# Kernel optimization log

Measured on AMD Instinct MI355X. Metric: run time of the kernel, lower is better.

## Reference

```python
import jax, jax.numpy as jnp
import numpy as np

N = 50000      # nodes
E = 800000     # directed edges (before self-loops)
IN = 128       # in_channels
H = 4          # heads (layers 1,2)
C = 64         # hidden_channels per head
OUT = 512      # out_channels of final Linear
LEAKY_SLOPE = 0.2


def _gat_layer(x, src, dst, n, W, a_src, a_dst, b, concat):
    """PyG GATConv (v1): shared linear, additive attention, segment softmax over dst."""
    heads, ch = a_src.shape
    xl = (x @ W).reshape(n, heads, ch)                       # [N,H,C]
    as_n = jnp.sum(xl * a_src, axis=-1)                      # [N,H] alpha_src per node
    ad_n = jnp.sum(xl * a_dst, axis=-1)                      # [N,H] alpha_dst per node
    logits = jax.nn.leaky_relu(as_n[src] + ad_n[dst], LEAKY_SLOPE)  # [Etot,H]
    m = jax.lax.stop_gradient(jax.ops.segment_max(logits, dst, num_segments=n))
    p = jnp.exp(logits - m[dst])
    denom = jax.ops.segment_sum(p, dst, num_segments=n) + 1e-16
    alpha = p / denom[dst]                                   # segment softmax over incoming edges
    out = jax.ops.segment_sum(xl[src] * alpha[:, :, None], dst, num_segments=n)  # [N,H,C]
    out = out.reshape(n, heads * ch) if concat else out.mean(axis=1)
    return out + b


def setup_inputs() -> dict:
    key = jax.random.key(0)
    ks = jax.random.split(key, 16)

    def gl(k, shape, fan_in):
        return jax.random.normal(k, shape, dtype=jnp.float32) * np.float32(1.0 / np.sqrt(fan_in))

    x = jax.random.normal(ks[0], (N, IN), dtype=jnp.float32)
    edge_index = jax.random.randint(ks[1], (2, E), 0, N, dtype=jnp.int32)

    inp = {
        "x": x,
        "edge_index": edge_index,
        # layer 1: in -> H*C (concat)
        "W1": gl(ks[2], (IN, H * C), IN),
        "a_src1": gl(ks[3], (H, C), C),
        "a_dst1": gl(ks[4], (H, C), C),
        "b1": jnp.zeros((H * C,), jnp.float32),
        # layer 2: H*C -> H*C (concat)
        "W2": gl(ks[5], (H * C, H * C), H * C),
        "a_src2": gl(ks[6], (H, C), C),
        "a_dst2": gl(ks[7], (H, C), C),
        "b2": jnp.zeros((H * C,), jnp.float32),
        # layer 3: H*C -> C (1 head, no concat)
        "W3": gl(ks[8], (H * C, C), H * C),
        "a_src3": gl(ks[9], (1, C), C),
        "a_dst3": gl(ks[10], (1, C), C),
        "b3": jnp.zeros((C,), jnp.float32),
        # final fc: C -> OUT
        "Wfc": gl(ks[11], (C, OUT), C),
        "bfc": jnp.zeros((OUT,), jnp.float32),
    }
    return inp


def reference(x, edge_index, W1, a_src1, a_dst1, b1, W2, a_src2, a_dst2, b2,
              W3, a_src3, a_dst3, b3, Wfc, bfc):
    n = x.shape[0]
    loop = jnp.arange(n, dtype=edge_index.dtype)             # PyG GATConv adds self-loops
    src = jnp.concatenate([edge_index[0], loop])
    dst = jnp.concatenate([edge_index[1], loop])

    h = jax.nn.relu(_gat_layer(x, src, dst, n, W1, a_src1, a_dst1, b1, True))
    h = jax.nn.relu(_gat_layer(h, src, dst, n, W2, a_src2, a_dst2, b2, True))
    h = jax.nn.relu(_gat_layer(h, src, dst, n, W3, a_src3, a_dst3, b3, False))
    return jax.nn.relu(h @ Wfc + bfc)                        # [N, OUT]
```

## Files before the change

kernel.cpp:

```cpp
#include <hip/hip_runtime.h>
#include <cstdint>
#include <cstddef>

typedef unsigned short ushort_t;
typedef __bf16 bf16x8 __attribute__((ext_vector_type(8)));
typedef float f32x4 __attribute__((ext_vector_type(4)));

__device__ __forceinline__ float b2f(ushort_t u) {
    return __uint_as_float(((unsigned int)u) << 16);
}
__device__ __forceinline__ ushort_t f2b(float f) {
    __bf16 h = (__bf16)f;
    return *(ushort_t*)&h;
}
__device__ __forceinline__ float lo16(unsigned int u) { return __uint_as_float(u << 16); }
__device__ __forceinline__ float hi16(unsigned int u) { return __uint_as_float(u & 0xffff0000u); }
__device__ __forceinline__ unsigned int pack2(float a, float b) {
    return ((unsigned int)f2b(b) << 16) | (unsigned int)f2b(a);
}

__device__ __forceinline__ void stage8(const float* __restrict__ g, ushort_t* s) {
    float4 f0 = *(const float4*)g;
    float4 f1 = *(const float4*)(g + 4);
    union { ushort_t u[8]; uint4 v; } t;
    t.u[0] = f2b(f0.x); t.u[1] = f2b(f0.y); t.u[2] = f2b(f0.z); t.u[3] = f2b(f0.w);
    t.u[4] = f2b(f1.x); t.u[5] = f2b(f1.y); t.u[6] = f2b(f1.z); t.u[7] = f2b(f1.w);
    *(uint4*)s = t.v;
}
__device__ __forceinline__ void stage8(const ushort_t* __restrict__ g, ushort_t* s) {
    *(float4*)s = *(const float4*)g;
}

__device__ __forceinline__ void tr_seg(int id, const float* __restrict__ W,
                                       ushort_t* __restrict__ WT, int K, int N2) {
    int n = id / K, k = id - n * K;
    WT[id] = f2b(W[k * N2 + n]);
}
__global__ __launch_bounds__(256) void transpose_all_kernel(const float* __restrict__ W1,
                                                            const float* __restrict__ W2,
                                                            const float* __restrict__ W3,
                                                            const float* __restrict__ Wfc,
                                                            ushort_t* __restrict__ W1T,
                                                            ushort_t* __restrict__ W2T,
                                                            ushort_t* __restrict__ W3T,
                                                            ushort_t* __restrict__ WfcT) {
    int id = blockIdx.x * 256 + threadIdx.x;
    if (id < 32768) { tr_seg(id, W1, W1T, 128, 256); return; }
    id -= 32768;
    if (id < 65536) { tr_seg(id, W2, W2T, 256, 256); return; }
    id -= 65536;
    if (id < 16384) { tr_seg(id, W3, W3T, 256, 64); return; }
    id -= 16384;
    if (id < 32768) { tr_seg(id, Wfc, WfcT, 64, 512); return; }
}

__global__ __launch_bounds__(256) void degree_kernel(const int* __restrict__ ei_dst,
                                                     int* __restrict__ deg, int E, int Etot) {
    int e = blockIdx.x * 256 + threadIdx.x;
    if (e >= Etot) return;
    int d = (e < E) ? ei_dst[e] : (e - E);
    atomicAdd(&deg[d], 1);
}

__global__ __launch_bounds__(256) void partial_sum_kernel(const int* __restrict__ deg,
                                                          int* __restrict__ bsum, int n) {
    __shared__ int ws[4];
    int t = threadIdx.x;
    int i = blockIdx.x * 256 + t;
    int v = (i < n) ? deg[i] : 0;
#pragma unroll
    for (int off = 32; off; off >>= 1) v += __shfl_xor(v, off, 64);
    if ((t & 63) == 0) ws[t >> 6] = v;
    __syncthreads();
    if (t == 0) bsum[blockIdx.x] = ws[0] + ws[1] + ws[2] + ws[3];
}

__global__ __launch_bounds__(256) void scan_bsum_kernel(const int* __restrict__ bsum,
                                                        int* __restrict__ boff,
                                                        int* __restrict__ rowoff,
                                                        int nblk, int n) {
    __shared__ int sm[256];
    int t = threadIdx.x;
    int v = (t < nblk) ? bsum[t] : 0;
    sm[t] = v;
    __syncthreads();
#pragma unroll
    for (int off = 1; off < 256; off <<= 1) {
        int u = (t >= off) ? sm[t - off] : 0;
        __syncthreads();
        sm[t] += u;
        __syncthreads();
    }
    if (t < nblk) boff[t] = sm[t] - v;
    if (t == 255) rowoff[n] = sm[255];
}

__global__ __launch_bounds__(256) void block_scan_kernel(const int* __restrict__ deg,
                                                         const int* __restrict__ boff,
                                                         int* __restrict__ rowoff,
                                                         int* __restrict__ cursor, int n) {
    __shared__ int sm[256];
    int t = threadIdx.x;
    int i = blockIdx.x * 256 + t;
    int v = (i < n) ? deg[i] : 0;
    sm[t] = v;
    __syncthreads();
#pragma unroll
    for (int off = 1; off < 256; off <<= 1) {
        int u = (t >= off) ? sm[t - off] : 0;
        __syncthreads();
        sm[t] += u;
        __syncthreads();
    }
    if (i < n) {
        int r = boff[blockIdx.x] + sm[t] - v;
        rowoff[i] = r;
        cursor[i] = r;
    }
}

__global__ __launch_bounds__(256) void scatter_kernel(const int* __restrict__ ei_src,
                                                      const int* __restrict__ ei_dst,
                                                      int* __restrict__ cursor,
                                                      int* __restrict__ ssrc, int E, int Etot) {
    int e = blockIdx.x * 256 + threadIdx.x;
    if (e >= Etot) return;
    int s, d;
    if (e < E) { s = ei_src[e]; d = ei_dst[e]; } else { s = d = e - E; }
    int pos = atomicAdd(&cursor[d], 1);
    ssrc[pos] = s;
}

template <typename TA, int NB, int EPI>
__global__ __launch_bounds__(256) void gemm_mfma(const TA* __restrict__ A,
                                                 const ushort_t* __restrict__ WT,
                                                 float* __restrict__ C,
                                                 ushort_t* __restrict__ Cb,
                                                 const float* __restrict__ bias,
                                                 int M, int K, int N2) {
    __shared__ ushort_t sA[64 * 32];
    __shared__ ushort_t sB[NB * 32];
    const int tid = threadIdx.x;
    const int wv = tid >> 6, lane = tid & 63;
    const int quad = lane >> 4, l16 = lane & 15;
    const int bm = blockIdx.x * 64, bn = blockIdx.y * NB;
    const int srow = tid >> 2, skof = (tid & 3) * 8;
    f32x4 acc[NB / 16] = {};

    for (int k0 = 0; k0 < K; k0 += 32) {
        int gm = bm + srow;
        gm = gm < M ? gm : M - 1;
        stage8(A + (size_t)gm * K + k0 + skof, sA + srow * 32 + skof);
#pragma unroll
        for (int r = 0; r < NB / 64; r++) {
            int brow = r * 64 + srow;
            stage8(WT + (size_t)(bn + brow) * K + k0 + skof, sB + brow * 32 + skof);
        }
        __syncthreads();

        bf16x8 af = *(const bf16x8*)(sA + (wv * 16 + l16) * 32 + quad * 8);
#pragma unroll
        for (int j = 0; j < NB / 16; j++) {
            bf16x8 bf = *(const bf16x8*)(sB + (j * 16 + l16) * 32 + quad * 8);
            acc[j] = __builtin_amdgcn_mfma_f32_16x16x32_bf16(af, bf, acc[j], 0, 0, 0);
        }
        __syncthreads();
    }

#pragma unroll
    for (int j = 0; j < NB / 16; j++) {
        int col = bn + j * 16 + l16;
        float bv = (EPI != 0) ? bias[col] : 0.f;
#pragma unroll
        for (int r = 0; r < 4; r++) {
            int row = bm + wv * 16 + quad * 4 + r;
            if (row < M) {
                float v = acc[j][r];
                if (EPI == 1) {
                    v += bv;
                    v = v > 0.f ? v : 0.f;
                    C[(size_t)row * N2 + col] = v;
                } else {
                    Cb[(size_t)row * N2 + col] = f2b(v);
                }
            }
        }
    }
}

template <int CH>
__global__ __launch_bounds__(256) void attn_kernel(const ushort_t* __restrict__ xl,
                                                   const float* __restrict__ a_src,
                                                   const float* __restrict__ a_dst,
                                                   float* __restrict__ as_n,
                                                   float* __restrict__ ad_n, int N) {
    int n = blockIdx.x * 4 + (threadIdx.x >> 6);
    int lane = threadIdx.x & 63;
    if (n >= N) return;
    if (CH == 256) {
        ushort4 u = ((const ushort4*)xl)[(size_t)n * 64 + lane];
        float4 av = ((const float4*)a_src)[lane];
        float4 dv = ((const float4*)a_dst)[lane];
        float x0 = b2f(u.x), x1 = b2f(u.y), x2 = b2f(u.z), x3 = b2f(u.w);
        float s = x0 * av.x + x1 * av.y + x2 * av.z + x3 * av.w;
        float d = x0 * dv.x + x1 * dv.y + x2 * dv.z + x3 * dv.w;
#pragma unroll
        for (int off = 8; off; off >>= 1) {
            s += __shfl_xor(s, off, 64);
            d += __shfl_xor(d, off, 64);
        }
        if ((lane & 15) == 0) {
            int h = lane >> 4;
            as_n[n * 4 + h] = s;
            ad_n[n * 4 + h] = d;
        }
    } else {
        float xv = b2f(xl[(size_t)n * 64 + lane]);
        float s = xv * a_src[lane];
        float d = xv * a_dst[lane];
#pragma unroll
        for (int off = 32; off; off >>= 1) {
            s += __shfl_xor(s, off, 64);
            d += __shfl_xor(d, off, 64);
        }
        if (lane == 0) { as_n[n] = s; ad_n[n] = d; }
    }
}

template <int CH>
__global__ __launch_bounds__(256) void aggregate_kernel(const ushort_t* __restrict__ xl,
                                                        const float* __restrict__ as_n,
                                                        const float* __restrict__ ad_n,
                                                        const int* __restrict__ rowoff,
                                                        const int* __restrict__ ssrc,
                                                        const float* __restrict__ bias,
                                                        ushort_t* __restrict__ hout, int N) {
    const int tid = threadIdx.x;
    const int wv = tid >> 6, lane = tid & 63;
    const uint4* xv = (const uint4*)xl;
    if (CH == 256) {
        const int hw = lane >> 5, l32 = lane & 31;
        const int dd = blockIdx.x * 8 + wv * 2 + hw;
        if (dd >= N) return;
        const int h = l32 >> 3;
        const int r0 = rowoff[dd], r1 = rowoff[dd + 1];
        const float adv = ad_n[dd * 4 + h];
        float a0 = 0, a1 = 0, a2 = 0, a3 = 0, a4 = 0, a5 = 0, a6 = 0, a7 = 0, den = 0;
        for (int i = r0; i < r1; i += 8) {
            int s[8];
            float g[8];
            uint4 u[8];
#pragma unroll
            for (int j = 0; j < 8; j++) {
                int t = i + j;
                s[j] = ssrc[t < r1 ? t : r0];
            }
#pragma unroll
            for (int j = 0; j < 8; j++) g[j] = as_n[s[j] * 4 + h];
#pragma unroll
            for (int j = 0; j < 8; j++) u[j] = xv[(size_t)s[j] * 32 + l32];
#pragma unroll
            for (int j = 0; j < 8; j++) {
                float lg = g[j] + adv;
                lg = lg > 0.f ? lg : 0.2f * lg;
                float p = (i + j < r1) ? __expf(lg) : 0.f;
                den += p;
                a0 += p * lo16(u[j].x); a1 += p * hi16(u[j].x);
                a2 += p * lo16(u[j].y); a3 += p * hi16(u[j].y);
                a4 += p * lo16(u[j].z); a5 += p * hi16(u[j].z);
                a6 += p * lo16(u[j].w); a7 += p * hi16(u[j].w);
            }
        }
        float di = 1.f / (den + 1e-16f);
        float4 b0 = ((const float4*)bias)[l32 * 2];
        float4 b1 = ((const float4*)bias)[l32 * 2 + 1];
        float v0 = a0 * di + b0.x, v1 = a1 * di + b0.y;
        float v2 = a2 * di + b0.z, v3 = a3 * di + b0.w;
        float v4 = a4 * di + b1.x, v5 = a5 * di + b1.y;
        float v6 = a6 * di + b1.z, v7 = a7 * di + b1.w;
        v0 = v0 > 0.f ? v0 : 0.f; v1 = v1 > 0.f ? v1 : 0.f;
        v2 = v2 > 0.f ? v2 : 0.f; v3 = v3 > 0.f ? v3 : 0.f;
        v4 = v4 > 0.f ? v4 : 0.f; v5 = v5 > 0.f ? v5 : 0.f;
        v6 = v6 > 0.f ? v6 : 0.f; v7 = v7 > 0.f ? v7 : 0.f;
        uint4 o;
        o.x = pack2(v0, v1); o.y = pack2(v2, v3);
        o.z = pack2(v4, v5); o.w = pack2(v6, v7);
        ((uint4*)hout)[(size_t)dd * 32 + l32] = o;
    } else {
        const int grp = lane >> 3, l8 = lane & 7;
        const int dd = blockIdx.x * 32 + wv * 8 + grp;
        if (dd >= N) return;
        const int r0 = rowoff[dd], r1 = rowoff[dd + 1];
        const float adv = ad_n[dd];
        float a0 = 0, a1 = 0, a2 = 0, a3 = 0, a4 = 0, a5 = 0, a6 = 0, a7 = 0, den = 0;
        for (int i = r0; i < r1; i += 8) {
            int s[8];
            float g[8];
            uint4 u[8];
#pragma unroll
            for (int j = 0; j < 8; j++) {
                int t = i + j;
                s[j] = ssrc[t < r1 ? t : r0];
            }
#pragma unroll
            for (int j = 0; j < 8; j++) g[j] = as_n[s[j]];
#pragma unroll
            for (int j = 0; j < 8; j++) u[j] = xv[(size_t)s[j] * 8 + l8];
#pragma unroll
            for (int j = 0; j < 8; j++) {
                float lg = g[j] + adv;
                lg = lg > 0.f ? lg : 0.2f * lg;
                float p = (i + j < r1) ? __expf(lg) : 0.f;
                den += p;
                a0 += p * lo16(u[j].x); a1 += p * hi16(u[j].x);
                a2 += p * lo16(u[j].y); a3 += p * hi16(u[j].y);
                a4 += p * lo16(u[j].z); a5 += p * hi16(u[j].z);
                a6 += p * lo16(u[j].w); a7 += p * hi16(u[j].w);
            }
        }
        float di = 1.f / (den + 1e-16f);
        float4 b0 = ((const float4*)bias)[l8 * 2];
        float4 b1 = ((const float4*)bias)[l8 * 2 + 1];
        float v0 = a0 * di + b0.x, v1 = a1 * di + b0.y;
        float v2 = a2 * di + b0.z, v3 = a3 * di + b0.w;
        float v4 = a4 * di + b1.x, v5 = a5 * di + b1.y;
        float v6 = a6 * di + b1.z, v7 = a7 * di + b1.w;
        v0 = v0 > 0.f ? v0 : 0.f; v1 = v1 > 0.f ? v1 : 0.f;
        v2 = v2 > 0.f ? v2 : 0.f; v3 = v3 > 0.f ? v3 : 0.f;
        v4 = v4 > 0.f ? v4 : 0.f; v5 = v5 > 0.f ? v5 : 0.f;
        v6 = v6 > 0.f ? v6 : 0.f; v7 = v7 > 0.f ? v7 : 0.f;
        uint4 o;
        o.x = pack2(v0, v1); o.y = pack2(v2, v3);
        o.z = pack2(v4, v5); o.w = pack2(v6, v7);
        ((uint4*)hout)[(size_t)dd * 8 + l8] = o;
    }
}

extern "C" void kernel_launch(void* const* d_in, const int* in_sizes, int n_in,
                              void* d_out, int out_size, void* d_ws, size_t ws_size,
                              hipStream_t stream) {
    const int N = in_sizes[0] / 128;
    const int E = in_sizes[1] / 2;
    const int Etot = E + N;

    const float* x = (const float*)d_in[0];
    const int* ei = (const int*)d_in[1];
    const int* ei_src = ei;
    const int* ei_dst = ei + E;
    float* out = (float*)d_out;

    const float* as1 = (const float*)d_in[3];
    const float* ad1 = (const float*)d_in[4];
    const float* b1  = (const float*)d_in[5];
    const float* as2 = (const float*)d_in[7];
    const float* ad2 = (const float*)d_in[8];
    const float* b2  = (const float*)d_in[9];
    const float* as3 = (const float*)d_in[11];
    const float* ad3 = (const float*)d_in[12];
    const float* b3  = (const float*)d_in[13];
    const float* bfc = (const float*)d_in[15];

    ushort_t* bufX = (ushort_t*)d_ws;
    ushort_t* bufH = bufX + (size_t)N * 256;
    ushort_t* W1T  = bufH + (size_t)N * 256;
    ushort_t* W2T  = W1T + 32768;
    ushort_t* W3T  = W2T + 65536;
    ushort_t* WfcT = W3T + 16384;
    float* asn = (float*)(WfcT + 32768);
    float* adn = asn + (size_t)N * 4;
    int* deg    = (int*)(adn + (size_t)N * 4);
    int* rowoff = deg + N;
    int* cursor = rowoff + N + 1;
    int* ssrc   = cursor + N;
    int* bsum   = ssrc + Etot;
    int* boff   = bsum + 256;

    transpose_all_kernel<<<576, 256, 0, stream>>>((const float*)d_in[2], (const float*)d_in[6],
                                                  (const float*)d_in[10], (const float*)d_in[14],
                                                  W1T, W2T, W3T, WfcT);

    hipMemsetAsync(deg, 0, (size_t)N * sizeof(int), stream);
    int eb = (Etot + 255) / 256;
    degree_kernel<<<eb, 256, 0, stream>>>(ei_dst, deg, E, Etot);
    const int NBLK = (N + 255) / 256;
    partial_sum_kernel<<<NBLK, 256, 0, stream>>>(deg, bsum, N);
    scan_bsum_kernel<<<1, 256, 0, stream>>>(bsum, boff, rowoff, NBLK, N);
    block_scan_kernel<<<NBLK, 256, 0, stream>>>(deg, boff, rowoff, cursor, N);
    scatter_kernel<<<eb, 256, 0, stream>>>(ei_src, ei_dst, cursor, ssrc, E, Etot);

    const int MB = (N + 63) / 64;
    int nb4 = (N + 3) / 4;
    int nb8 = (N + 7) / 8;
    int nb32 = (N + 31) / 32;

    gemm_mfma<float, 256, 0><<<dim3(MB, 1), 256, 0, stream>>>(x, W1T, nullptr, bufX, nullptr, N, 128, 256);
    attn_kernel<256><<<nb4, 256, 0, stream>>>(bufX, as1, ad1, asn, adn, N);
    aggregate_kernel<256><<<nb8, 256, 0, stream>>>(bufX, asn, adn, rowoff, ssrc, b1, bufH, N);

    gemm_mfma<ushort_t, 256, 0><<<dim3(MB, 1), 256, 0, stream>>>(bufH, W2T, nullptr, bufX, nullptr, N, 256, 256);
    attn_kernel<256><<<nb4, 256, 0, stream>>>(bufX, as2, ad2, asn, adn, N);
    aggregate_kernel<256><<<nb8, 256, 0, stream>>>(bufX, asn, adn, rowoff, ssrc, b2, bufH, N);

    gemm_mfma<ushort_t, 64, 0><<<dim3(MB, 1), 256, 0, stream>>>(bufH, W3T, nullptr, bufX, nullptr, N, 256, 64);
    attn_kernel<64><<<nb4, 256, 0, stream>>>(bufX, as3, ad3, asn, adn, N);
    aggregate_kernel<64><<<nb32, 256, 0, stream>>>(bufX, asn, adn, rowoff, ssrc, b3, bufH, N);

    gemm_mfma<ushort_t, 256, 1><<<dim3(MB, 2), 256, 0, stream>>>(bufH, WfcT, out, nullptr, bfc, N, 64, 512);
}
```

Baseline: 521.6 us.

## Use 128x128 MFMA GEMM tiles and pre-convert x to bf16

Replaces the 64xNB GEMM, where each wave computed one 16-row strip, with a 128x128 tile kernel in which each wave owns a 64x64 sub-tile of 4x4 MFMA accumulators. This raises register-level reuse of the A and B fragments. It also adds a separate pass that converts x to bf16 once, so the GEMM loads only bf16, and hoists pointer arithmetic out of the K loop. The costs are an extra kernel launch plus a write and read of the bf16 copy of x, and higher register use per thread, which may lower occupancy.

```diff
diff --git a/kernel.cpp b/kernel.cpp
--- a/kernel.cpp
+++ b/kernel.cpp
@@ -17,18 +17,6 @@
 __device__ __forceinline__ float hi16(unsigned int u) { return __uint_as_float(u & 0xffff0000u); }
 __device__ __forceinline__ unsigned int pack2(float a, float b) {
     return ((unsigned int)f2b(b) << 16) | (unsigned int)f2b(a);
-}
-
-__device__ __forceinline__ void stage8(const float* __restrict__ g, ushort_t* s) {
-    float4 f0 = *(const float4*)g;
-    float4 f1 = *(const float4*)(g + 4);
-    union { ushort_t u[8]; uint4 v; } t;
-    t.u[0] = f2b(f0.x); t.u[1] = f2b(f0.y); t.u[2] = f2b(f0.z); t.u[3] = f2b(f0.w);
-    t.u[4] = f2b(f1.x); t.u[5] = f2b(f1.y); t.u[6] = f2b(f1.z); t.u[7] = f2b(f1.w);
-    *(uint4*)s = t.v;
-}
-__device__ __forceinline__ void stage8(const ushort_t* __restrict__ g, ushort_t* s) {
-    *(float4*)s = *(const float4*)g;
 }
 
 __device__ __forceinline__ void tr_seg(int id, const float* __restrict__ W,
@@ -54,6 +42,19 @@
     if (id < 32768) { tr_seg(id, Wfc, WfcT, 64, 512); return; }
 }
 
+__global__ __launch_bounds__(256) void xb_kernel(const float* __restrict__ x,
+                                                 ushort_t* __restrict__ xb, int total8) {
+    int id = blockIdx.x * 256 + threadIdx.x;
+    if (id >= total8) return;
+    const float* g = x + (size_t)id * 8;
+    float4 f0 = *(const float4*)g;
+    float4 f1 = *(const float4*)(g + 4);
+    uint4 o;
+    o.x = pack2(f0.x, f0.y); o.y = pack2(f0.z, f0.w);
+    o.z = pack2(f1.x, f1.y); o.w = pack2(f1.z, f1.w);
+    ((uint4*)xb)[id] = o;
+}
+
 __global__ __launch_bounds__(256) void degree_kernel(const int* __restrict__ ei_dst,
                                                      int* __restrict__ deg, int E, int Etot) {
     int e = blockIdx.x * 256 + threadIdx.x;
@@ -131,36 +132,103 @@
     ssrc[pos] = s;
 }
 
-template <typename TA, int NB, int EPI>
-__global__ __launch_bounds__(256) void gemm_mfma(const TA* __restrict__ A,
-                                                 const ushort_t* __restrict__ WT,
-                                                 float* __restrict__ C,
-                                                 ushort_t* __restrict__ Cb,
-                                                 const float* __restrict__ bias,
-                                                 int M, int K, int N2) {
+template <int EPI>
+__global__ __launch_bounds__(256) void gemm128_mfma(const ushort_t* __restrict__ A,
+                                                    const ushort_t* __restrict__ WT,
+                                                    float* __restrict__ C,
+                                                    ushort_t* __restrict__ Cb,
+                                                    const float* __restrict__ bias,
+                                                    int M, int K, int N2) {
+    __shared__ ushort_t sA[128 * 32];
+    __shared__ ushort_t sB[128 * 32];
+    const int tid = threadIdx.x;
+    const int wv = tid >> 6, lane = tid & 63;
+    const int wr = wv >> 1, wc = wv & 1;
+    const int quad = lane >> 4, l16 = lane & 15;
+    const int bm = blockIdx.x * 128, bn = blockIdx.y * 128;
+    const int sr0 = tid >> 2, sc = (tid & 3) * 8;
+    const int sr1 = sr0 + 64;
+    f32x4 acc[4][4] = {};
+
+    int ga0 = bm + sr0; ga0 = ga0 < M ? ga0 : M - 1;
+    int ga1 = bm + sr1; ga1 = ga1 < M ? ga1 : M - 1;
+    const ushort_t* pa0 = A + (size_t)ga0 * K + sc;
+    const ushort_t* pa1 = A + (size_t)ga1 * K + sc;
+    const ushort_t* pb0 = WT + (size_t)(bn + sr0) * K + sc;
+    const ushort_t* pb1 = WT + (size_t)(bn + sr1) * K + sc;
+
+    for (int k0 = 0; k0 < K; k0 += 32) {
+        *(float4*)(sA + sr0 * 32 + sc) = *(const float4*)(pa0 + k0);
+        *(float4*)(sA + sr1 * 32 + sc) = *(const float4*)(pa1 + k0);
+        *(float4*)(sB + sr0 * 32 + sc) = *(const float4*)(pb0 + k0);
+        *(float4*)(sB + sr1 * 32 + sc) = *(const float4*)(pb1 + k0);
+        __syncthreads();
+
+        bf16x8 af[4], bfr[4];
+#pragma unroll
+        for (int m = 0; m < 4; m++)
+            af[m] = *(const bf16x8*)(sA + (wr * 64 + m * 16 + l16) * 32 + quad * 8);
+#pragma unroll
+        for (int n = 0; n < 4; n++)
+            bfr[n] = *(const bf16x8*)(sB + (wc * 64 + n * 16 + l16) * 32 + quad * 8);
+#pragma unroll
+        for (int m = 0; m < 4; m++)
+#pragma unroll
+            for (int n = 0; n < 4; n++)
+                acc[m][n] = __builtin_amdgcn_mfma_f32_16x16x32_bf16(af[m], bfr[n], acc[m][n], 0, 0, 0);
+        __syncthreads();
+    }
+
+#pragma unroll
+    for (int n = 0; n < 4; n++) {
+        int col = bn + wc * 64 + n * 16 + l16;
+        float bv = (EPI == 1) ? bias[col] : 0.f;
+#pragma unroll
+        for (int m = 0; m < 4; m++) {
+#pragma unroll
+            for (int r = 0; r < 4; r++) {
+                int row = bm + wr * 64 + m * 16 + quad * 4 + r;
+                if (row < M) {
+                    float v = acc[m][n][r];
+                    if (EPI == 1) {
+                        v += bv;
+                        v = v > 0.f ? v : 0.f;
+                        C[(size_t)row * N2 + col] = v;
+                    } else {
+                        Cb[(size_t)row * N2 + col] = f2b(v);
+                    }
+                }
+            }
+        }
+    }
+}
+
+__global__ __launch_bounds__(256) void gemm64_mfma(const ushort_t* __restrict__ A,
+                                                   const ushort_t* __restrict__ WT,
+                                                   ushort_t* __restrict__ Cb,
+                                                   int M, int K, int N2) {
     __shared__ ushort_t sA[64 * 32];
-    __shared__ ushort_t sB[NB * 32];
+    __shared__ ushort_t sB[64 * 32];
     const int tid = threadIdx.x;
     const int wv = tid >> 6, lane = tid & 63;
     const int quad = lane >> 4, l16 = lane & 15;
-    const int bm = blockIdx.x * 64, bn = blockIdx.y * NB;
+    const int bm = blockIdx.x * 64;
     const int srow = tid >> 2, skof = (tid & 3) * 8;
-    f32x4 acc[NB / 16] = {};
+    f32x4 acc[4] = {};
+
+    int gm = bm + srow;
+    gm = gm < M ? gm : M - 1;
+    const ushort_t* pa = A + (size_t)gm * K + skof;
+    const ushort_t* pb = WT + (size_t)srow * K + skof;
 
     for (int k0 = 0; k0 < K; k0 += 32) {
-        int gm = bm + srow;
-        gm = gm < M ? gm : M - 1;
-        stage8(A + (size_t)gm * K + k0 + skof, sA + srow * 32 + skof);
-#pragma unroll
-        for (int r = 0; r < NB / 64; r++) {
-            int brow = r * 64 + srow;
-            stage8(WT + (size_t)(bn + brow) * K + k0 + skof, sB + brow * 32 + skof);
-        }
+        *(float4*)(sA + srow * 32 + skof) = *(const float4*)(pa + k0);
+        *(float4*)(sB + srow * 32 + skof) = *(const float4*)(pb + k0);
         __syncthreads();
 
         bf16x8 af = *(const bf16x8*)(sA + (wv * 16 + l16) * 32 + quad * 8);
 #pragma unroll
-        for (int j = 0; j < NB / 16; j++) {
+        for (int j = 0; j < 4; j++) {
             bf16x8 bf = *(const bf16x8*)(sB + (j * 16 + l16) * 32 + quad * 8);
             acc[j] = __builtin_amdgcn_mfma_f32_16x16x32_bf16(af, bf, acc[j], 0, 0, 0);
         }
@@ -168,22 +236,12 @@
     }
 
 #pragma unroll
-    for (int j = 0; j < NB / 16; j++) {
-        int col = bn + j * 16 + l16;
-        float bv = (EPI != 0) ? bias[col] : 0.f;
+    for (int j = 0; j < 4; j++) {
+        int col = j * 16 + l16;
 #pragma unroll
         for (int r = 0; r < 4; r++) {
             int row = bm + wv * 16 + quad * 4 + r;
-            if (row < M) {
-                float v = acc[j][r];
-                if (EPI == 1) {
-                    v += bv;
-                    v = v > 0.f ? v : 0.f;
-                    C[(size_t)row * N2 + col] = v;
-                } else {
-                    Cb[(size_t)row * N2 + col] = f2b(v);
-                }
-            }
+            if (row < M) Cb[(size_t)row * N2 + col] = f2b(acc[j][r]);
         }
     }
 }
@@ -374,10 +432,12 @@
     int* ssrc   = cursor + N;
     int* bsum   = ssrc + Etot;
     int* boff   = bsum + 256;
+    ushort_t* xb = (ushort_t*)(boff + 256);
 
     transpose_all_kernel<<<576, 256, 0, stream>>>((const float*)d_in[2], (const float*)d_in[6],
                                                   (const float*)d_in[10], (const float*)d_in[14],
                                                   W1T, W2T, W3T, WfcT);
+    xb_kernel<<<(N * 16 + 255) / 256, 256, 0, stream>>>(x, xb, N * 16);
 
     hipMemsetAsync(deg, 0, (size_t)N * sizeof(int), stream);
     int eb = (Etot + 255) / 256;
@@ -388,22 +448,23 @@
     block_scan_kernel<<<NBLK, 256, 0, stream>>>(deg, boff, rowoff, cursor, N);
     scatter_kernel<<<eb, 256, 0, stream>>>(ei_src, ei_dst, cursor, ssrc, E, Etot);
 
-    const int MB = (N + 63) / 64;
+    const int MB128 = (N + 127) / 128;
+    const int MB64 = (N + 63) / 64;
     int nb4 = (N + 3) / 4;
     int nb8 = (N + 7) / 8;
     int nb32 = (N + 31) / 32;
 
-    gemm_mfma<float, 256, 0><<<dim3(MB, 1), 256, 0, stream>>>(x, W1T, nullptr, bufX, nullptr, N, 128, 256);
+    gemm128_mfma<0><<<dim3(MB128, 2), 256, 0, stream>>>(xb, W1T, nullptr, bufX, nullptr, N, 128, 256);
     attn_kernel<256><<<nb4, 256, 0, stream>>>(bufX, as1, ad1, asn, adn, N);
     aggregate_kernel<256><<<nb8, 256, 0, stream>>>(bufX, asn, adn, rowoff, ssrc, b1, bufH, N);
 
-    gemm_mfma<ushort_t, 256, 0><<<dim3(MB, 1), 256, 0, stream>>>(bufH, W2T, nullptr, bufX, nullptr, N, 256, 256);
+    gemm128_mfma<0><<<dim3(MB128, 2), 256, 0, stream>>>(bufH, W2T, nullptr, bufX, nullptr, N, 256, 256);
     attn_kernel<256><<<nb4, 256, 0, stream>>>(bufX, as2, ad2, asn, adn, N);
     aggregate_kernel<256><<<nb8, 256, 0, stream>>>(bufX, asn, adn, rowoff, ssrc, b2, bufH, N);
 
-    gemm_mfma<ushort_t, 64, 0><<<dim3(MB, 1), 256, 0, stream>>>(bufH, W3T, nullptr, bufX, nullptr, N, 256, 64);
+    gemm64_mfma<<<dim3(MB64, 1), 256, 0, stream>>>(bufH, W3T, bufX, N, 256, 64);
     attn_kernel<64><<<nb4, 256, 0, stream>>>(bufX, as3, ad3, asn, adn, N);
     aggregate_kernel<64><<<nb32, 256, 0, stream>>>(bufX, asn, adn, rowoff, ssrc, b3, bufH, N);
 
-    gemm_mfma<ushort_t, 256, 1><<<dim3(MB, 2), 256, 0, stream>>>(bufH, WfcT, out, nullptr, bfc, N, 64, 512);
-}
+    gemm128_mfma<1><<<dim3(MB128, 4), 256, 0, stream>>>(bufH, WfcT, out, nullptr, bfc, N, 64, 512);
+}
```

Measured after the change: 505.2 us. 1.03x faster.
